# Kernel optimization log

Hardware: AMD Instinct MI355X
Metric: run time of the kernel (lower is better)

Reference implementation:

```python
import jax, jax.numpy as jnp
import numpy as np

EPS = 1e-15


def _trace(t):
    return jnp.einsum('bii->b', t)


def _ortho_loss(ss, k):
    n = jnp.linalg.norm(ss, axis=(-1, -2), keepdims=True)
    diff = ss / n - jnp.eye(k, dtype=ss.dtype) / np.float32(np.sqrt(k))
    return jnp.mean(jnp.linalg.norm(diff, axis=(-1, -2)))


def _mincut_terms(s, adj):
    out_adj = jnp.einsum('bnk,bnm,bml->bkl', s, adj, s)
    d_flat = adj.sum(-1)  # degrees [B,N]
    num = _trace(out_adj)
    den = _trace(jnp.einsum('bnk,bn,bnl->bkl', s, d_flat, s)) + EPS
    return out_adj, num, den, d_flat


def dense_mincut_rewiring(x, adj, s, mask):
    k = s.shape[-1]  # 2
    m = mask[..., None].astype(x.dtype)
    s = jax.nn.softmax(s, axis=-1) * m
    _, num, den, _ = _mincut_terms(s, adj)
    mincut_loss = -jnp.mean(num / den)
    ortho_loss = _ortho_loss(jnp.einsum('bnk,bnl->bkl', s, s), k)
    # laplacian derivative of spectral gap wrt A_uv: (f_u - f_v)^2, f = soft bipartition
    f = s[..., 0]
    dlam = (f[:, :, None] - f[:, None, :]) ** 2
    return adj * (1.0 - dlam), mincut_loss, ortho_loss


def dense_CT_rewiring(x, adj, s, mask):
    k = s.shape[-1]
    m = mask[..., None].astype(x.dtype)
    s = jax.nn.softmax(s, axis=-1) * m
    d_flat = adj.sum(-1)
    sds = _trace(jnp.einsum('bnk,bn,bnl->bkl', s, d_flat, s))
    sas = _trace(jnp.einsum('bnk,bnm,bml->bkl', s, adj, s))
    den = _trace(jnp.einsum('bnk,bnl->bkl', s, s)) + EPS
    ct_loss = jnp.mean((sds - sas) / den)  # tr(Z^T L Z) / tr(Z^T Z)
    ortho_loss = _ortho_loss(jnp.einsum('bnk,bnl->bkl', s, s), k)
    # pairwise CT distances ||z_u - z_v|| / vol(G), sparsified by A
    sq = (s * s).sum(-1)
    d2 = sq[:, :, None] + sq[:, None, :] - 2.0 * jnp.einsum('bnk,bmk->bnm', s, s)
    ct_dist = jnp.sqrt(jnp.maximum(d2, 0.0) + 1e-12)
    vol = d_flat.sum(-1)
    new_adj = (ct_dist / (vol[:, None, None] + EPS)) * adj
    return new_adj, ct_loss, ortho_loss


def dense_mincut_pool(x, adj, s, mask):
    k = s.shape[-1]
    m = mask[..., None].astype(x.dtype)
    s = jax.nn.softmax(s, axis=-1) * m
    x = x * m
    out = jnp.einsum('bnk,bnf->bkf', s, x)
    out_adj, num, den, _ = _mincut_terms(s, adj)
    mincut_loss = -jnp.mean(num / den)
    ortho_loss = _ortho_loss(jnp.einsum('bnk,bnl->bkl', s, s), k)
    out_adj = out_adj * (1.0 - jnp.eye(k, dtype=adj.dtype))  # zero diagonal
    d = jnp.sqrt(out_adj.sum(-1)) + EPS  # [B,k]
    out_adj = out_adj / d[:, None, :] / d[:, :, None]
    return out, out_adj, mincut_loss, ortho_loss


def _dgc(x, adj, w_rel, b_rel, w_root):
    # DenseGraphConv(aggr='add'): lin_rel(A @ x) + lin_root(x)
    return jnp.matmul(adj, x) @ w_rel + b_rel + x @ w_root


def setup_inputs() -> dict:
    B, N, IN, H, KC, OUT, KMC = 16, 1024, 128, 32, 32, 10, 16
    keys = iter(jax.random.split(jax.random.key(0), 48))

    def lin(fin, fout):
        lim = float(1.0 / np.sqrt(fin))
        return (jax.random.uniform(next(keys), (fin, fout), jnp.float32, -lim, lim),
                jax.random.uniform(next(keys), (fout,), jnp.float32, -lim, lim))

    x = jax.random.normal(next(keys), (B, N, IN), jnp.float32)
    u = jax.random.uniform(next(keys), (B, N, N), jnp.float32)
    a = (u < 0.0156).astype(jnp.float32)  # avg degree ~16
    adj = jnp.maximum(a, jnp.swapaxes(a, 1, 2)) * (1.0 - jnp.eye(N, dtype=jnp.float32))
    mask = jnp.ones((B, N), dtype=bool)
    W1, b1 = lin(IN, H)
    Wrw, brw = lin(H, 2)
    Wg_rel, bg = lin(H, H); Wg_root, _ = lin(H, H)
    Wmcg, bmcg = lin(H, KMC)
    W2g_rel, b2g = lin(H, H); W2g_root, _ = lin(H, H)
    Wct, bct = lin(H, KC)
    Wc_rel, bc = lin(H, H); Wc_root, _ = lin(H, H)
    Wmcc, bmcc = lin(H, KMC)
    Wcat, bcat = lin(2 * H, H)
    W2, b2 = lin(H, H)
    W3, b3 = lin(H, OUT)
    return dict(x=x, adj=adj, mask=mask, W1=W1, b1=b1, Wrw=Wrw, brw=brw,
                Wg_rel=Wg_rel, bg=bg, Wg_root=Wg_root, Wmcg=Wmcg, bmcg=bmcg,
                W2g_rel=W2g_rel, b2g=b2g, W2g_root=W2g_root, Wct=Wct, bct=bct,
                Wc_rel=Wc_rel, bc=bc, Wc_root=Wc_root, Wmcc=Wmcc, bmcc=bmcc,
                Wcat=Wcat, bcat=bcat, W2=W2, b2=b2, W3=W3, b3=b3)


def reference(x, adj, mask, W1, b1, Wrw, brw, Wg_rel, bg, Wg_root, Wmcg, bmcg,
              W2g_rel, b2g, W2g_root, Wct, bct, Wc_rel, bc, Wc_root, Wmcc, bmcc,
              Wcat, bcat, W2, b2, W3, b3):
    x = x @ W1 + b1
    # GAP branch
    adj_gap, mc_rw, ol_rw = dense_mincut_rewiring(x, adj, x @ Wrw + brw, mask)
    x_gap = _dgc(x, adj_gap, Wg_rel, bg, Wg_root)
    x_gap, adj_gap, mc1, ol1 = dense_mincut_pool(x_gap, adj_gap, x_gap @ Wmcg + bmcg, mask)
    x_gap = _dgc(x_gap, adj_gap, W2g_rel, b2g, W2g_root)
    # CT branch
    adj_ct, ct_loss, ol_ct = dense_CT_rewiring(x, adj, x @ Wct + bct, mask)
    x_ct = _dgc(x, adj_ct, Wc_rel, bc, Wc_root)
    x_ct, adj_ct, mc2, ol2 = dense_mincut_pool(x_ct, adj_ct, x_ct @ Wmcc + bmcc, mask)
    x_ct = _dgc(x_ct, adj_ct, W2g_rel, b2g, W2g_root)  # source reuses self.conv2gap here
    h = jax.nn.relu(jnp.concatenate([x_gap, x_ct], axis=2) @ Wcat + bcat).sum(axis=1)
    h = jax.nn.relu(h @ W2 + b2)
    logits = h @ W3 + b3
    main_loss = mc_rw + ct_loss + mc1 + mc2
    ortho_loss = ol_rw + ol_ct + ol1 + ol2
    return (jax.nn.log_softmax(logits, axis=-1), main_loss, ortho_loss)
```

## Files before the change

### kernel.cpp

```cpp
#include <hip/hip_runtime.h>
#include <math.h>

#define BB   16
#define NNODE 1024
#define INF_ 128
#define HH   32
#define KMC  16
#define CAP  128
#define EPS15 1e-15f

typedef float v4f __attribute__((ext_vector_type(4)));

#define OFF_X      0
#define OFF_SRW    524288
#define OFF_SQCT   557056
#define OFF_SCT    573440
#define OFF_D      1097728
#define OFF_NUMRW  1114112
#define OFF_SAS    1130496
#define OFF_DGAP   1146880
#define OFF_DCT    1163264
#define OFF_YGAP   1179648
#define OFF_YCT    1703936
#define OFF_XGAP   2228224
#define OFF_XCT    2752512
#define OFF_S2G    3276800
#define OFF_S2C    3538944
#define OFF_TG     3801088
#define OFF_TC     4063232
#define OFF_FROB   4325376
#define OFF_VOL    4325888
#define OFF_MCRW   4325904
#define OFF_CTB    4325920
#define OFF_OLRW   4325936
#define OFF_OLCT   4325952
#define OFF_MC1    4325968
#define OFF_MC2    4325984
#define OFF_OL1    4326000
#define OFF_OL2    4326016
#define OFF_OUTG   4326032
#define OFF_OUTC   4334224
#define OFF_G2G    4342416
#define OFF_G2C    4346512
#define OFF_OAG    4350608
#define OFF_OAC    4354704
#define OFF_ENNZ   4358800
#define OFF_EIDX   4375184
#define OFF_EWG    5423760
#define OFF_EWC    7520912
#define WS_NEED    9618064

__device__ __forceinline__ float wave_sum(float v) {
#pragma unroll
  for (int off = 32; off >= 1; off >>= 1) v += __shfl_xor(v, off, 64);
  return v;
}

__device__ __forceinline__ float blk_sum(float v, float* sred, int tid) {
  v = wave_sum(v);
  __syncthreads();
  if ((tid & 63) == 0) sred[tid >> 6] = v;
  __syncthreads();
  return sred[0] + sred[1] + sred[2] + sred[3];
}

__global__ __launch_bounds__(256) void k_fused0(
    const float* __restrict__ adj, const float* __restrict__ x,
    const float* __restrict__ W1, const float* __restrict__ b1,
    const float* __restrict__ Wrw, const float* __restrict__ brw,
    const float* __restrict__ Wct, const float* __restrict__ bct,
    float* __restrict__ ws)
{
  __shared__ float sW1[INF_*HH];
  __shared__ float sWct[HH*HH];
  __shared__ float sWrw[HH*2];
  __shared__ float sb1[HH], sbct[HH], sbrw[2];
  __shared__ float sx[8*INF_];
  __shared__ float sX[8*HH];
  __shared__ unsigned int s_e32[4][2][CAP/2];
  int tid = threadIdx.x;
  if (blockIdx.x < 2048) {
    int w = tid >> 6, lane = tid & 63;
    int row0 = blockIdx.x * 8 + w * 2;
    const v4f* a0 = (const v4f*)(adj + (size_t)row0 * NNODE);
    const v4f* a1 = (const v4f*)(adj + (size_t)(row0 + 1) * NNODE);
    v4f v[8];
#pragma unroll
    for (int it = 0; it < 4; it++) v[it]     = __builtin_nontemporal_load(&a0[it*64 + lane]);
#pragma unroll
    for (int it = 0; it < 4; it++) v[4 + it] = __builtin_nontemporal_load(&a1[it*64 + lane]);
#pragma unroll
    for (int rr = 0; rr < 2; rr++) {
      int row = row0 + rr;
      int c = 0;
#pragma unroll
      for (int it = 0; it < 4; it++) {
        v4f a4 = v[rr*4 + it];
        c += (a4.x != 0.f) + (a4.y != 0.f) + (a4.z != 0.f) + (a4.w != 0.f);
      }
      int p = c;
#pragma unroll
      for (int off = 1; off < 64; off <<= 1) {
        int t = __shfl_up(p, off, 64);
        if (lane >= off) p += t;
      }
      int excl = p - c;
      int total = __shfl(p, 63, 64);
      unsigned short* es = (unsigned short*)s_e32[w][rr];
      int pos = excl;
#pragma unroll
      for (int it = 0; it < 4; it++) {
        v4f a4 = v[rr*4 + it];
        int m0 = it*256 + lane*4;
        if (a4.x != 0.f) { if (pos < CAP) es[pos] = (unsigned short)(m0+0); pos++; }
        if (a4.y != 0.f) { if (pos < CAP) es[pos] = (unsigned short)(m0+1); pos++; }
        if (a4.z != 0.f) { if (pos < CAP) es[pos] = (unsigned short)(m0+2); pos++; }
        if (a4.w != 0.f) { if (pos < CAP) es[pos] = (unsigned short)(m0+3); pos++; }
      }
      int nnzc = total < CAP ? total : CAP;
      __syncthreads();
      unsigned int* dst = (unsigned int*)((unsigned short*)(ws + OFF_EIDX) + (size_t)row*CAP);
      int n32 = (nnzc + 1) >> 1;
      if (lane < n32) dst[lane] = s_e32[w][rr][lane];
      if (lane == 0) {
        ((int*)(ws + OFF_ENNZ))[row] = nnzc;
        ws[OFF_D + row] = (float)total;
      }
    }
  } else {
    for (int i = tid; i < INF_*HH; i += 256) sW1[i] = W1[i];
    for (int i = tid; i < HH*HH; i += 256) sWct[i] = Wct[i];
    if (tid < HH*2) sWrw[tid] = Wrw[tid];
    if (tid < HH) { sb1[tid] = b1[tid]; sbct[tid] = bct[tid]; }
    if (tid < 2) sbrw[tid] = brw[tid];
    size_t row0 = (size_t)(blockIdx.x - 2048) * 8;
    ((float4*)sx)[tid] = ((const float4*)(x + row0 * INF_))[tid];
    __syncthreads();
    int r = tid >> 5, h = tid & 31;
    float acc = sb1[h];
#pragma unroll 8
    for (int k = 0; k < INF_; k++) acc += sx[r*INF_ + k] * sW1[k*HH + h];
    size_t row = row0 + r;
    ws[OFF_X + row*HH + h] = acc;
    sX[r*HH + h] = acc;
    __syncthreads();
    float sraw = sbct[h];
#pragma unroll
    for (int k = 0; k < HH; k++) sraw += sX[r*HH + k] * sWct[k*HH + h];
    float mx = sraw;
#pragma unroll
    for (int off = 16; off >= 1; off >>= 1) mx = fmaxf(mx, __shfl_xor(mx, off, 32));
    float e = __expf(sraw - mx);
    float sum = e;
#pragma unroll
    for (int off = 16; off >= 1; off >>= 1) sum += __shfl_xor(sum, off, 32);
    float sv = e / sum;
    ws[OFF_SCT + row*HH + h] = sv;
    float sq = sv * sv;
#pragma unroll
    for (int off = 16; off >= 1; off >>= 1) sq += __shfl_xor(sq, off, 32);
    float xv = sX[r*HH + h];
    float t0 = xv * sWrw[h*2 + 0];
    float t1 = xv * sWrw[h*2 + 1];
#pragma unroll
    for (int off = 16; off >= 1; off >>= 1) { t0 += __shfl_xor(t0, off, 32); t1 += __shfl_xor(t1, off, 32); }
    if (h == 0) {
      ws[OFF_SQCT + row] = sq;
      float r0 = t0 + sbrw[0], r1 = t1 + sbrw[1];
      float m2 = fmaxf(r0, r1);
      float e0 = __expf(r0 - m2), e1 = __expf(r1 - m2);
      float inv = 1.0f / (e0 + e1);
      ((float2*)(ws + OFF_SRW))[row] = make_float2(e0*inv, e1*inv);
    }
  }
}

__global__ __launch_bounds__(256) void k_edge(float* __restrict__ ws)
{
  __shared__ int   s_m[4][CAP];
  __shared__ float s_wg[4][CAP];
  __shared__ float s_wc[4][CAP];
  __shared__ float sp[8][32];
  int tid = threadIdx.x;
  if (blockIdx.x < 4096) {
    const float* X = ws + OFF_X;
    const float2* srw = (const float2*)(ws + OFF_SRW);
    const float* sqct = ws + OFF_SQCT;
    const float* sct = ws + OFF_SCT;
    int w = tid >> 6, lane = tid & 63;
    int row = blockIdx.x * 4 + w;
    int b = row >> 10;
    int nnz = ((const int*)(ws + OFF_ENNZ))[row];
    const unsigned short* eidx = (const unsigned short*)(ws + OFF_EIDX) + (size_t)row*CAP;
    const float4* cn4 = (const float4*)(sct + (size_t)row * HH);
    float4 c[8];
#pragma unroll
    for (int i = 0; i < 8; i++) c[i] = cn4[i];
    float2 srwn = srw[row];
    float f_n = srwn.x;
    float sq_n = sqct[row];
    float numrw_p = 0.f, sas_p = 0.f, dg_p = 0.f, dc_p = 0.f;
    for (int e = lane; e < nnz; e += 64) {
      int m = eidx[e];
      s_m[w][e] = m;
      const float4* cm4 = (const float4*)(sct + ((size_t)b*NNODE + m) * HH);
      float dot = 0.f;
#pragma unroll
      for (int i = 0; i < 8; i++) {
        float4 d4 = cm4[i];
        dot += c[i].x*d4.x + c[i].y*d4.y + c[i].z*d4.z + c[i].w*d4.w;
      }
      float2 srwm = srw[b*NNODE + m];
      numrw_p += srwn.x*srwm.x + srwn.y*srwm.y;
      float df = f_n - srwm.x;
      float wg = 1.0f - df*df;
      float d2 = sq_n + sqct[b*NNODE + m] - 2.0f*dot;
      float wc = sqrtf(fmaxf(d2, 0.0f) + 1e-12f);
      sas_p += dot;
      dg_p += wg;
      dc_p += wc;
      s_wg[w][e] = wg;
      s_wc[w][e] = wc;
      size_t eo = (size_t)row*CAP + e;
      ws[OFF_EWG + eo] = wg;
      ws[OFF_EWC + eo] = wc;
    }
    float numrw = wave_sum(numrw_p);
    float sas = wave_sum(sas_p);
    float dgp = wave_sum(dg_p);
    float dcp = wave_sum(dc_p);
    if (lane == 0) {
      ws[OFF_NUMRW + row] = numrw;
      ws[OFF_SAS + row] = sas;
      ws[OFF_DGAP + row] = dgp;
      ws[OFF_DCT + row] = dcp;
    }
    __syncthreads();
    int eoff = lane >> 4, hp = lane & 15;
    float yg0 = 0.f, yg1 = 0.f, yc0 = 0.f, yc1 = 0.f;
    for (int e = eoff; e < nnz; e += 4) {
      int m = s_m[w][e];
      float wg = s_wg[w][e], wc = s_wc[w][e];
      float2 xv = ((const float2*)(X + ((size_t)b*NNODE + m)*HH))[hp];
      yg0 += wg*xv.x; yg1 += wg*xv.y;
      yc0 += wc*xv.x; yc1 += wc*xv.y;
    }
    yg0 += __shfl_xor(yg0, 16, 64); yg0 += __shfl_xor(yg0, 32, 64);
    yg1 += __shfl_xor(yg1, 16, 64); yg1 += __shfl_xor(yg1, 32, 64);
    yc0 += __shfl_xor(yc0, 16, 64); yc0 += __shfl_xor(yc0, 32, 64);
    yc1 += __shfl_xor(yc1, 16, 64); yc1 += __shfl_xor(yc1, 32, 64);
    if (eoff == 0) {
      ((float2*)(ws + OFF_YGAP + (size_t)row*HH))[hp] = make_float2(yg0, yg1);
      ((float2*)(ws + OFF_YCT  + (size_t)row*HH))[hp] = make_float2(yc0, yc1);
    }
  } else {
    int blk = blockIdx.x - 4096;
    int b = blk >> 5, i = blk & 31;
    const float* sct = ws + OFF_SCT + (size_t)b*NNODE*HH;
    int j = tid & 31, seg = tid >> 5;
    float acc = 0.f;
    for (int n = seg*128; n < seg*128 + 128; n++)
      acc += sct[n*HH + i] * sct[n*HH + j];
    sp[seg][j] = acc;
    __syncthreads();
    if (tid < 32) {
      float g = 0.f;
#pragma unroll
      for (int s = 0; s < 8; s++) g += sp[s][tid];
      float p = g * g;
#pragma unroll
      for (int off = 16; off >= 1; off >>= 1) p += __shfl_xor(p, off, 32);
      if (tid == 0) ws[OFF_FROB + blk] = p;
    }
  }
}

__global__ __launch_bounds__(256) void k_batch1(float* __restrict__ ws)
{
  __shared__ float sred[4];
  int b = blockIdx.x, tid = threadIdx.x;
  for (int i = tid; i < 2048; i += 256) ws[OFF_OUTG + b*2048 + i] = 0.f;
  size_t base = (size_t)b * NNODE;
  const float2* srw = (const float2*)(ws + OFF_SRW);
  float vol_p=0, denrw_p=0, num_p=0, sds_p=0, sas_p=0, denct_p=0, g00_p=0, g01_p=0, g11_p=0;
  for (int n = tid; n < NNODE; n += 256) {
    float d = ws[OFF_D + base + n];
    float2 s = srw[base + n];
    float sq = ws[OFF_SQCT + base + n];
    vol_p += d;
    denrw_p += d * (s.x*s.x + s.y*s.y);
    num_p += ws[OFF_NUMRW + base + n];
    sds_p += d * sq;
    sas_p += ws[OFF_SAS + base + n];
    denct_p += sq;
    g00_p += s.x*s.x; g01_p += s.x*s.y; g11_p += s.y*s.y;
  }
  float frob_p = (tid < 32) ? ws[OFF_FROB + b*32 + tid] : 0.f;
  float vol = blk_sum(vol_p, sred, tid);
  float denrw = blk_sum(denrw_p, sred, tid);
  float num = blk_sum(num_p, sred, tid);
  float sds = blk_sum(sds_p, sred, tid);
  float sas = blk_sum(sas_p, sred, tid);
  float denct = blk_sum(denct_p, sred, tid);
  float g00 = blk_sum(g00_p, sred, tid);
  float g01 = blk_sum(g01_p, sred, tid);
  float g11 = blk_sum(g11_p, sred, tid);
  float frob2 = blk_sum(frob_p, sred, tid);
  if (tid == 0) {
    ws[OFF_VOL + b] = vol;
    ws[OFF_MCRW + b] = -num / (denrw + EPS15);
    ws[OFF_CTB + b] = (sds - sas) / (denct + EPS15);
    float nrw = sqrtf(g00*g00 + 2.f*g01*g01 + g11*g11);
    ws[OFF_OLRW + b] = sqrtf(fmaxf(2.f - 2.f*(g00 + g11)/(nrw*1.41421356237f), 0.f));
    float nct = sqrtf(frob2);
    ws[OFF_OLCT + b] = sqrtf(fmaxf(2.f - 2.f*denct/(nct*5.65685424949f), 0.f));
  }
}

__global__ __launch_bounds__(256) void k_feat(
    const float* __restrict__ Wg_rel, const float* __restrict__ bg, const float* __restrict__ Wg_root,
    const float* __restrict__ Wc_rel, const float* __restrict__ bc, const float* __restrict__ Wc_root,
    const float* __restrict__ Wmcg, const float* __restrict__ bmcg,
    const float* __restrict__ Wmcc, const float* __restrict__ bmcc,
    float* __restrict__ ws)
{
  __shared__ float sWgrel[HH*HH], sWgroot[HH*HH], sWcrel[HH*HH], sWcroot[HH*HH];
  __shared__ float sWmcg[HH*KMC], sWmcc[HH*KMC];
  __shared__ float sbg[HH], sbc[HH], sbmcg[KMC], sbmcc[KMC];
  __shared__ float syg[8*HH], syc[8*HH], sXl[8*HH], sxg[8*HH], sxc[8*HH];
  int tid = threadIdx.x;
  for (int i = tid; i < HH*HH; i += 256) {
    sWgrel[i] = Wg_rel[i]; sWgroot[i] = Wg_root[i];
    sWcrel[i] = Wc_rel[i]; sWcroot[i] = Wc_root[i];
  }
  for (int i = tid; i < HH*KMC; i += 256) { sWmcg[i] = Wmcg[i]; sWmcc[i] = Wmcc[i]; }
  if (tid < HH) { sbg[tid] = bg[tid]; sbc[tid] = bc[tid]; }
  if (tid < KMC) { sbmcg[tid] = bmcg[tid]; sbmcc[tid] = bmcc[tid]; }
  size_t row0 = (size_t)blockIdx.x * 8;
  int b = (int)(row0 >> 10);
  syg[tid] = ws[OFF_YGAP + row0*HH + tid];
  syc[tid] = ws[OFF_YCT + row0*HH + tid];
  sXl[tid] = ws[OFF_X + row0*HH + tid];
  __syncthreads();
  float ivol = 1.0f / (ws[OFF_VOL + b] + EPS15);
  int r = tid >> 5, h = tid & 31;
  float accg = 0.f, accg2 = 0.f, accc = 0.f, accc2 = 0.f;
#pragma unroll
  for (int k = 0; k < HH; k++) {
    float ygv = syg[r*HH + k], Xv = sXl[r*HH + k], ycv = syc[r*HH + k];
    accg  += ygv * sWgrel[k*HH + h];
    accg2 += Xv  * sWgroot[k*HH + h];
    accc  += ycv * sWcrel[k*HH + h];
    accc2 += Xv  * sWcroot[k*HH + h];
  }
  float xgv = sbg[h] + accg + accg2;
  float xcv = sbc[h] + ivol*accc + accc2;
  size_t row = row0 + r;
  ws[OFF_XGAP + row*HH + h] = xgv;
  ws[OFF_XCT + row*HH + h] = xcv;
  sxg[r*HH + h] = xgv;
  sxc[r*HH + h] = xcv;
  __syncthreads();
  int j = h & 15, halfsel = h >> 4;
  const float* sin_ = halfsel ? sxc : sxg;
  const float* sw = halfsel ? sWmcc : sWmcg;
  float raw = halfsel ? sbmcc[j] : sbmcg[j];
#pragma unroll
  for (int k = 0; k < HH; k++) raw += sin_[r*HH + k] * sw[k*KMC + j];
  float mx = raw;
#pragma unroll
  for (int off = 8; off >= 1; off >>= 1) mx = fmaxf(mx, __shfl_xor(mx, off, 16));
  float e = __expf(raw - mx);
  float sum = e;
#pragma unroll
  for (int off = 8; off >= 1; off >>= 1) sum += __shfl_xor(sum, off, 16);
  float sv = e / sum;
  if (halfsel == 0) ws[OFF_S2G + row*KMC + j] = sv;
  else              ws[OFF_S2C + row*KMC + j] = sv;
}

__global__ __launch_bounds__(256) void k_pass2c(float* __restrict__ ws)
{
  int tid = threadIdx.x;
  int w = tid >> 6, lane = tid & 63;
  (void)w;
  int row = blockIdx.x * 4 + (tid >> 6);
  int b = row >> 10;
  int nnz = ((const int*)(ws + OFF_ENNZ))[row];
  const unsigned short* eidx = (const unsigned short*)(ws + OFF_EIDX) + (size_t)row*CAP;
  int grp = lane >> 5;
  int el  = lane & 31;
  const float* ew = ws + (grp ? OFF_EWC : OFF_EWG) + (size_t)row*CAP;
  const float* S2 = ws + (grp ? OFF_S2C : OFF_S2G) + (size_t)b*NNODE*KMC;
  float acc[16];
#pragma unroll
  for (int i = 0; i < 16; i++) acc[i] = 0.f;
  for (int e = el; e < nnz; e += 32) {
    int m = eidx[e];
    float wv = ew[e];
    const float4* p = (const float4*)(S2 + m*KMC);
    float4 q0 = p[0], q1 = p[1], q2 = p[2], q3 = p[3];
    acc[0] += wv*q0.x; acc[1] += wv*q0.y; acc[2]  += wv*q0.z; acc[3]  += wv*q0.w;
    acc[4] += wv*q1.x; acc[5] += wv*q1.y; acc[6]  += wv*q1.z; acc[7]  += wv*q1.w;
    acc[8] += wv*q2.x; acc[9] += wv*q2.y; acc[10] += wv*q2.z; acc[11] += wv*q2.w;
    acc[12]+= wv*q3.x; acc[13]+= wv*q3.y; acc[14] += wv*q3.z; acc[15] += wv*q3.w;
  }
#pragma unroll
  for (int off = 1; off < 32; off <<= 1) {
#pragma unroll
    for (int i = 0; i < 16; i++) acc[i] += __shfl_xor(acc[i], off, 32);
  }
  if (el == 0) {
    float* tp = ws + (grp ? OFF_TC : OFF_TG) + (size_t)row*KMC;
#pragma unroll
    for (int i = 0; i < 4; i++)
      ((float4*)tp)[i] = make_float4(acc[4*i], acc[4*i+1], acc[4*i+2], acc[4*i+3]);
  }
}

__global__ __launch_bounds__(256) void k_red2(float* __restrict__ ws)
{
  __shared__ float sg[64*16], sc[64*16], stg[64*16], stc[64*16];
  __shared__ float sxg[64*32], sxc[64*32];
  int b = blockIdx.x >> 4, chunk = blockIdx.x & 15;
  int tid = threadIdx.x;
  size_t n0 = (size_t)b * NNODE + chunk * 64;
  const float* pG  = ws + OFF_S2G  + n0 * KMC;
  const float* pC  = ws + OFF_S2C  + n0 * KMC;
  const float* pTG = ws + OFF_TG   + n0 * KMC;
  const float* pTC = ws + OFF_TC   + n0 * KMC;
  const float* pXG = ws + OFF_XGAP + n0 * HH;
  const float* pXC = ws + OFF_XCT  + n0 * HH;
#pragma unroll
  for (int i = 0; i < 4; i++) {
    sg [tid + i*256] = pG [tid + i*256];
    sc [tid + i*256] = pC [tid + i*256];
    stg[tid + i*256] = pTG[tid + i*256];
    stc[tid + i*256] = pTC[tid + i*256];
  }
#pragma unroll
  for (int i = 0; i < 8; i++) {
    sxg[tid + i*256] = pXG[tid + i*256];
    sxc[tid + i*256] = pXC[tid + i*256];
  }
  __syncthreads();
  int k0 = tid >> 5, h0 = tid & 31;
  float og0 = 0.f, og1 = 0.f, oc0 = 0.f, oc1 = 0.f;
#pragma unroll 8
  for (int r = 0; r < 64; r++) {
    float xgv = sxg[r*32 + h0], xcv = sxc[r*32 + h0];
    og0 += sg[r*16 + k0]     * xgv;
    og1 += sg[r*16 + k0 + 8] * xgv;
    oc0 += sc[r*16 + k0]     * xcv;
    oc1 += sc[r*16 + k0 + 8] * xcv;
  }
  atomicAdd(&ws[OFF_OUTG + b*512 + k0*32 + h0],       og0);
  atomicAdd(&ws[OFF_OUTG + b*512 + (k0+8)*32 + h0],   og1);
  atomicAdd(&ws[OFF_OUTC + b*512 + k0*32 + h0],       oc0);
  atomicAdd(&ws[OFF_OUTC + b*512 + (k0+8)*32 + h0],   oc1);
  int k = tid >> 4, l = tid & 15;
  float gg = 0.f, gc = 0.f, ag = 0.f, ac = 0.f;
#pragma unroll 8
  for (int r = 0; r < 64; r++) {
    float sgk = sg[r*16 + k], sck = sc[r*16 + k];
    gg += sgk * sg [r*16 + l];
    gc += sck * sc [r*16 + l];
    ag += sgk * stg[r*16 + l];
    ac += sck * stc[r*16 + l];
  }
  atomicAdd(&ws[OFF_G2G + b*256 + tid], gg);
  atomicAdd(&ws[OFF_G2C + b*256 + tid], gc);
  atomicAdd(&ws[OFF_OAG + b*256 + tid], ag);
  atomicAdd(&ws[OFF_OAC + b*256 + tid], ac);
}

__global__ __launch_bounds__(256) void k_batch2(
    const float* __restrict__ W2g_rel, const float* __restrict__ b2g, const float* __restrict__ W2g_root,
    const float* __restrict__ Wcat, const float* __restrict__ bcat,
    const float* __restrict__ W2, const float* __restrict__ b2,
    const float* __restrict__ W3, const float* __restrict__ b3,
    float* __restrict__ out, float* __restrict__ ws)
{
  __shared__ float sOAg[256], sOAc[256], sOutg[512], sOutc[512];
  __shared__ float sW2grel[1024], sW2groot[1024], sWcat[2048], sW2l[1024];
  __shared__ float sPg[512], sPc[512], sXg2[512], sXc2[512], sHt[512];
  __shared__ float sHs[32], sH2[32], sLg[16], sScal[2];
  __shared__ float sdkg[16], sdkc[16];
  __shared__ float sred[4];
  int b = blockIdx.x, tid = threadIdx.x;
  sOAg[tid] = ws[OFF_OAG + b*256 + tid];
  sOAc[tid] = ws[OFF_OAC + b*256 + tid];
  sOutg[tid] = ws[OFF_OUTG + b*512 + tid];
  sOutg[tid + 256] = ws[OFF_OUTG + b*512 + tid + 256];
  sOutc[tid] = ws[OFF_OUTC + b*512 + tid];
  sOutc[tid + 256] = ws[OFF_OUTC + b*512 + tid + 256];
  for (int i = tid; i < 1024; i += 256) { sW2grel[i] = W2g_rel[i]; sW2groot[i] = W2g_root[i]; sW2l[i] = W2[i]; }
  for (int i = tid; i < 2048; i += 256) sWcat[i] = Wcat[i];
  size_t base = (size_t)b * NNODE;
  float den1_p = 0, den2_p = 0, trg_p = 0, trc_p = 0;
  for (int n = tid; n < NNODE; n += 256) {
    float dg = ws[OFF_DGAP + base + n], dc = ws[OFF_DCT + base + n];
    const float* pg = ws + OFF_S2G + (base + n)*KMC;
    const float* pc = ws + OFF_S2C + (base + n)*KMC;
    float ng = 0.f, nc = 0.f;
#pragma unroll
    for (int j = 0; j < KMC; j++) { ng += pg[j]*pg[j]; nc += pc[j]*pc[j]; }
    den1_p += dg * ng; den2_p += dc * nc; trg_p += ng; trc_p += nc;
  }
  float den1 = blk_sum(den1_p, sred, tid);
  float den2u = blk_sum(den2_p, sred, tid);
  float trg = blk_sum(trg_p, sred, tid);
  float trc = blk_sum(trc_p, sred, tid);
  float gv = ws[OFF_G2G + b*256 + tid];
  float cv = ws[OFF_G2C + b*256 + tid];
  float frobg2 = blk_sum(gv*gv, sred, tid);
  float frobc2 = blk_sum(cv*cv, sred, tid);
  float t1_p = (tid < 16) ? sOAg[tid*17] : 0.f;
  float t2_p = (tid < 16) ? sOAc[tid*17] : 0.f;
  float num1 = blk_sum(t1_p, sred, tid);
  float num2u = blk_sum(t2_p, sred, tid);
  float vol = ws[OFF_VOL + b];
  float ivol = 1.0f / (vol + EPS15);
  if (tid == 0) {
    ws[OFF_MC1 + b] = -num1 / (den1 + EPS15);
    ws[OFF_MC2 + b] = -(num2u*ivol) / (den2u*ivol + EPS15);
    ws[OFF_OL1 + b] = sqrtf(fmaxf(2.f - 2.f*trg/(sqrtf(frobg2)*4.f), 0.f));
    ws[OFF_OL2 + b] = sqrtf(fmaxf(2.f - 2.f*trc/(sqrtf(frobc2)*4.f), 0.f));
  }
  sOAc[tid] *= ivol;
  __syncthreads();
  if (tid < 16) { sOAg[tid*17] = 0.f; sOAc[tid*17] = 0.f; }
  __syncthreads();
  if (tid < 16) {
    float rg = 0.f, rc = 0.f;
#pragma unroll
    for (int l = 0; l < 16; l++) { rg += sOAg[tid*16 + l]; rc += sOAc[tid*16 + l]; }
    sdkg[tid] = sqrtf(rg) + EPS15;
    sdkc[tid] = sqrtf(rc) + EPS15;
  }
  __syncthreads();
  { int k = tid >> 4, l = tid & 15;
    sOAg[tid] /= (sdkg[k]*sdkg[l]);
    sOAc[tid] /= (sdkc[k]*sdkc[l]); }
  __syncthreads();
  { int k = tid >> 5, h = tid & 31;
    float p0 = 0, p1 = 0, q0 = 0, q1 = 0;
#pragma unroll
    for (int l = 0; l < 16; l++) {
      p0 += sOAg[k*16 + l] * sOutg[l*32 + h];
      p1 += sOAg[(k+8)*16 + l] * sOutg[l*32 + h];
      q0 += sOAc[k*16 + l] * sOutc[l*32 + h];
      q1 += sOAc[(k+8)*16 + l] * sOutc[l*32 + h];
    }
    sPg[k*32 + h] = p0; sPg[(k+8)*32 + h] = p1;
    sPc[k*32 + h] = q0; sPc[(k+8)*32 + h] = q1;
  }
  __syncthreads();
  { int k = tid >> 5, h = tid & 31;
    float bb2 = b2g[h];
    float a0 = bb2, a1 = bb2, c0 = bb2, c1 = bb2;
#pragma unroll
    for (int q = 0; q < 32; q++) {
      float wr = sW2grel[q*32 + h], wo = sW2groot[q*32 + h];
      a0 += sPg[k*32 + q]*wr + sOutg[k*32 + q]*wo;
      a1 += sPg[(k+8)*32 + q]*wr + sOutg[(k+8)*32 + q]*wo;
      c0 += sPc[k*32 + q]*wr + sOutc[k*32 + q]*wo;
      c1 += sPc[(k+8)*32 + q]*wr + sOutc[(k+8)*32 + q]*wo;
    }
    sXg2[k*32 + h] = a0; sXg2[(k+8)*32 + h] = a1;
    sXc2[k*32 + h] = c0; sXc2[(k+8)*32 + h] = c1;
  }
  __syncthreads();
  { int k = tid >> 5, h = tid & 31;
    float bb = bcat[h];
    float t0 = bb, t1 = bb;
#pragma unroll
    for (int q = 0; q < 32; q++) {
      float w1v = sWcat[q*32 + h], w2v = sWcat[(q+32)*32 + h];
      t0 += sXg2[k*32 + q]*w1v + sXc2[k*32 + q]*w2v;
      t1 += sXg2[(k+8)*32 + q]*w1v + sXc2[(k+8)*32 + q]*w2v;
    }
    sHt[k*32 + h] = fmaxf(t0, 0.f);
    sHt[(k+8)*32 + h] = fmaxf(t1, 0.f);
  }
  __syncthreads();
  if (tid < 32) {
    float s = 0.f;
#pragma unroll
    for (int k = 0; k < 16; k++) s += sHt[k*32 + tid];
    sHs[tid] = s;
  }
  __syncthreads();
  if (tid < 32) {
    float a = b2[tid];
#pragma unroll
    for (int q = 0; q < 32; q++) a += sHs[q]*sW2l[q*32 + tid];
    sH2[tid] = fmaxf(a, 0.f);
  }
  __syncthreads();
  if (tid < 10) {
    float a = b3[tid];
#pragma unroll
    for (int q = 0; q < 32; q++) a += sH2[q]*W3[q*10 + tid];
    sLg[tid] = a;
  }
  __syncthreads();
  if (tid == 0) {
    float m = sLg[0];
    for (int o = 1; o < 10; o++) m = fmaxf(m, sLg[o]);
    float se = 0.f;
    for (int o = 0; o < 10; o++) se += __expf(sLg[o] - m);
    sScal[0] = m; sScal[1] = logf(se);
  }
  __syncthreads();
  if (tid < 10) out[b*10 + tid] = sLg[tid] - sScal[0] - sScal[1];
}

__global__ void k_loss(float* __restrict__ out, const float* __restrict__ ws)
{
  int t = threadIdx.x;
  float vm = 0.f, vo = 0.f;
  if (t < BB) {
    vm = ws[OFF_MCRW + t] + ws[OFF_CTB + t] + ws[OFF_MC1 + t] + ws[OFF_MC2 + t];
    vo = ws[OFF_OLRW + t] + ws[OFF_OLCT + t] + ws[OFF_OL1 + t] + ws[OFF_OL2 + t];
  }
  vm = wave_sum(vm);
  vo = wave_sum(vo);
  if (t == 0) { out[160] = vm / 16.f; out[161] = vo / 16.f; }
}

extern "C" void kernel_launch(void* const* d_in, const int* in_sizes, int n_in,
                              void* d_out, int out_size, void* d_ws, size_t ws_size,
                              hipStream_t stream)
{
  const float* x       = (const float*)d_in[0];
  const float* adj     = (const float*)d_in[1];
  const float* W1      = (const float*)d_in[3];
  const float* b1      = (const float*)d_in[4];
  const float* Wrw     = (const float*)d_in[5];
  const float* brw     = (const float*)d_in[6];
  const float* Wg_rel  = (const float*)d_in[7];
  const float* bg      = (const float*)d_in[8];
  const float* Wg_root = (const float*)d_in[9];
  const float* Wmcg    = (const float*)d_in[10];
  const float* bmcg    = (const float*)d_in[11];
  const float* W2g_rel = (const float*)d_in[12];
  const float* b2g     = (const float*)d_in[13];
  const float* W2g_root= (const float*)d_in[14];
  const float* Wct     = (const float*)d_in[15];
  const float* bct     = (const float*)d_in[16];
  const float* Wc_rel  = (const float*)d_in[17];
  const float* bc      = (const float*)d_in[18];
  const float* Wc_root = (const float*)d_in[19];
  const float* Wmcc    = (const float*)d_in[20];
  const float* bmcc    = (const float*)d_in[21];
  const float* Wcat    = (const float*)d_in[22];
  const float* bcat    = (const float*)d_in[23];
  const float* W2      = (const float*)d_in[24];
  const float* b2      = (const float*)d_in[25];
  const float* W3      = (const float*)d_in[26];
  const float* b3      = (const float*)d_in[27];
  float* out = (float*)d_out;
  float* ws  = (float*)d_ws;

  k_fused0<<<dim3(4096), dim3(256), 0, stream>>>(adj, x, W1, b1, Wrw, brw, Wct, bct, ws);
  k_edge<<<dim3(4608), dim3(256), 0, stream>>>(ws);
  k_batch1<<<dim3(16), dim3(256), 0, stream>>>(ws);
  k_feat<<<dim3(2048), dim3(256), 0, stream>>>(Wg_rel, bg, Wg_root, Wc_rel, bc, Wc_root,
                                               Wmcg, bmcg, Wmcc, bmcc, ws);
  k_pass2c<<<dim3(4096), dim3(256), 0, stream>>>(ws);
  k_red2<<<dim3(256), dim3(256), 0, stream>>>(ws);
  k_batch2<<<dim3(16), dim3(256), 0, stream>>>(W2g_rel, b2g, W2g_root, Wcat, bcat,
                                               W2, b2, W3, b3, out, ws);
  k_loss<<<dim3(1), dim3(64), 0, stream>>>(out, ws);
}
```

Baseline: 263.8 us.

## Remap edge blocks per XCD for L2 locality and pack per-node gather data

Blocks in the edge kernel, the Gram/Frobenius branch and pass2c are remapped so that each XCD (blockIdx & 7) works on two whole graphs. Per-graph node data then stays in that XCD's L2 instead of being spread across all eight. Per-node softmax weights and squared norms are also packed into one float4 buffer, so each edge gather needs one load instead of two. The cost is an extra 16-byte-per-node buffer appended to the workspace, and the WS_NEED define is replaced without a new size, which risks the workspace being under-allocated.

```diff
diff --git a/kernel.cpp b/kernel.cpp
--- a/kernel.cpp
+++ b/kernel.cpp
@@ -48,7 +48,7 @@
 #define OFF_EIDX   4375184
 #define OFF_EWG    5423760
 #define OFF_EWC    7520912
-#define WS_NEED    9618064
+#define OFF_PACK   9618064
 
 __device__ __forceinline__ float wave_sum(float v) {
 #pragma unroll
@@ -170,7 +170,9 @@
       float m2 = fmaxf(r0, r1);
       float e0 = __expf(r0 - m2), e1 = __expf(r1 - m2);
       float inv = 1.0f / (e0 + e1);
-      ((float2*)(ws + OFF_SRW))[row] = make_float2(e0*inv, e1*inv);
+      float s0 = e0*inv, s1 = e1*inv;
+      ((float2*)(ws + OFF_SRW))[row] = make_float2(s0, s1);
+      ((float4*)(ws + OFF_PACK))[row] = make_float4(s0, s1, sq, 0.f);
     }
   }
 }
@@ -183,13 +185,17 @@
   __shared__ float sp[8][32];
   int tid = threadIdx.x;
   if (blockIdx.x < 4096) {
+    int xcd = blockIdx.x & 7;
+    int idx = blockIdx.x >> 3;
+    int b = xcd*2 + (idx >> 8);
+    int chunk = idx & 255;
     const float* X = ws + OFF_X;
     const float2* srw = (const float2*)(ws + OFF_SRW);
     const float* sqct = ws + OFF_SQCT;
     const float* sct = ws + OFF_SCT;
+    const float4* pack = (const float4*)(ws + OFF_PACK) + (size_t)b*NNODE;
     int w = tid >> 6, lane = tid & 63;
-    int row = blockIdx.x * 4 + w;
-    int b = row >> 10;
+    int row = b*NNODE + chunk*4 + w;
     int nnz = ((const int*)(ws + OFF_ENNZ))[row];
     const unsigned short* eidx = (const unsigned short*)(ws + OFF_EIDX) + (size_t)row*CAP;
     const float4* cn4 = (const float4*)(sct + (size_t)row * HH);
@@ -210,11 +216,11 @@
         float4 d4 = cm4[i];
         dot += c[i].x*d4.x + c[i].y*d4.y + c[i].z*d4.z + c[i].w*d4.w;
       }
-      float2 srwm = srw[b*NNODE + m];
-      numrw_p += srwn.x*srwm.x + srwn.y*srwm.y;
-      float df = f_n - srwm.x;
+      float4 pk = pack[m];
+      numrw_p += srwn.x*pk.x + srwn.y*pk.y;
+      float df = f_n - pk.x;
       float wg = 1.0f - df*df;
-      float d2 = sq_n + sqct[b*NNODE + m] - 2.0f*dot;
+      float d2 = sq_n + pk.z - 2.0f*dot;
       float wc = sqrtf(fmaxf(d2, 0.0f) + 1e-12f);
       sas_p += dot;
       dg_p += wg;
@@ -255,7 +261,10 @@
     }
   } else {
     int blk = blockIdx.x - 4096;
-    int b = blk >> 5, i = blk & 31;
+    int xcd = blk & 7;
+    int idx = blk >> 3;
+    int b = xcd*2 + (idx >> 5);
+    int i = idx & 31;
     const float* sct = ws + OFF_SCT + (size_t)b*NNODE*HH;
     int j = tid & 31, seg = tid >> 5;
     float acc = 0.f;
@@ -270,7 +279,7 @@
       float p = g * g;
 #pragma unroll
       for (int off = 16; off >= 1; off >>= 1) p += __shfl_xor(p, off, 32);
-      if (tid == 0) ws[OFF_FROB + blk] = p;
+      if (tid == 0) ws[OFF_FROB + b*32 + i] = p;
     }
   }
 }
@@ -382,10 +391,12 @@
 __global__ __launch_bounds__(256) void k_pass2c(float* __restrict__ ws)
 {
   int tid = threadIdx.x;
-  int w = tid >> 6, lane = tid & 63;
-  (void)w;
-  int row = blockIdx.x * 4 + (tid >> 6);
-  int b = row >> 10;
+  int xcd = blockIdx.x & 7;
+  int idx = blockIdx.x >> 3;
+  int b = xcd*2 + (idx >> 8);
+  int chunk = idx & 255;
+  int row = b*NNODE + chunk*4 + (tid >> 6);
+  int lane = tid & 63;
   int nnz = ((const int*)(ws + OFF_ENNZ))[row];
   const unsigned short* eidx = (const unsigned short*)(ws + OFF_EIDX) + (size_t)row*CAP;
   int grp = lane >> 5;
```

New measurement: 262.4 us. Within noise of the previous version (-0.6%).
